# Performance work log

Hardware: AMD Instinct MI355X
Metric: run time of the kernel (lower is better)

Reference implementation:

```python
import jax, jax.numpy as jnp
import numpy as np


def setup_inputs() -> dict:
    key = jax.random.key(0)
    k1, k2 = jax.random.split(key)
    B, C, H = 1024, 1000, 512  # batch, classes, hidden
    y = jax.random.normal(k1, (B, C), dtype=jnp.float32)
    w = jax.random.normal(k2, (C, H), dtype=jnp.float32)
    epsilon = jnp.ones((), dtype=jnp.float32)
    lipschitz = jnp.ones((), dtype=jnp.float32)
    return {"y": y, "w": w, "epsilon": epsilon, "lipschitz": lipschitz}


def reference(y, w, epsilon, lipschitz):
    # y: [B, C] logits; w: [C, H] final-layer weight
    kW = lipschitz * w.T                      # [H, C]
    j = jnp.argmax(y, axis=1)                 # [B]
    y_j = jnp.max(y, axis=1, keepdims=True)   # [B, 1]
    kW_j = kW.T[j]                            # [B, H] gather of argmax column
    kW_ij = kW_j[:, :, None] - kW[None]       # [B, H, C] broadcast difference
    sq = jnp.sum(kW_ij * kW_ij, axis=1)       # [B, C]
    # safe sqrt (value identical; avoids NaN grad at the exact-zero j column)
    K_ij = jnp.where(sq > 0, jnp.sqrt(jnp.where(sq > 0, sq, 1.0)), 0.0)
    y_bot_i = y + epsilon * K_ij              # [B, C]
    y_bot_i = jnp.where(y == y_j, -jnp.inf, y_bot_i)
    y_bot = jnp.max(y_bot_i, axis=1, keepdims=True)  # [B, 1]
    return jnp.concatenate([y, y_bot], axis=1)       # [B, C+1]
```

## Files before the change

### kernel.cpp

```cpp
#include <hip/hip_runtime.h>
#include <math.h>

#define B_SZ 1024
#define C_SZ 1000
#define H_SZ 512


typedef __attribute__((ext_vector_type(8))) short bf16x8;
typedef __attribute__((ext_vector_type(4))) float f32x4;

#define KC 128
#define RS 136

__global__ __launch_bounds__(256) void k_prep(
    const float* __restrict__ y, const float* __restrict__ w,
    int* __restrict__ jv, float* __restrict__ ymax,
    float* __restrict__ wnorm, short* __restrict__ wbf,
    float* __restrict__ out) {
    const int r = blockIdx.x;
    const int tid = threadIdx.x;
    if (r < 250) {
        const int wave = tid >> 6, lane = tid & 63;
        const int c = r * 4 + wave;
        const float* row = w + c * H_SZ;
        float4 a = *(const float4*)(row + lane * 8);
        float4 b = *(const float4*)(row + lane * 8 + 4);
        float f[8] = {a.x, a.y, a.z, a.w, b.x, b.y, b.z, b.w};
        unsigned short u[8];
        float s = 0.f;
#pragma unroll
        for (int i = 0; i < 8; ++i) {
            s += f[i] * f[i];
            unsigned v = __float_as_uint(f[i]);
            v += 0x7fffu + ((v >> 16) & 1u);
            u[i] = (unsigned short)(v >> 16);
        }
        uint4 pk;
        pk.x = (unsigned)u[0] | ((unsigned)u[1] << 16);
        pk.y = (unsigned)u[2] | ((unsigned)u[3] << 16);
        pk.z = (unsigned)u[4] | ((unsigned)u[5] << 16);
        pk.w = (unsigned)u[6] | ((unsigned)u[7] << 16);
        *(uint4*)(wbf + c * H_SZ + lane * 8) = pk;
#pragma unroll
        for (int off = 32; off; off >>= 1) s += __shfl_down(s, off, 64);
        if (lane == 0) wnorm[c] = s;
    } else {
        const int b = r - 250;
        const float* yrow = y + b * C_SZ;
        float* orow = out + b * (C_SZ + 1);
        float best = -INFINITY;
        int bidx = 0x7fffffff;
        if (tid < 250) {
            float4 v = *(const float4*)(yrow + tid * 4);
            float e[4] = {v.x, v.y, v.z, v.w};
#pragma unroll
            for (int i = 0; i < 4; ++i) {
                orow[tid * 4 + i] = e[i];
                if (e[i] > best) { best = e[i]; bidx = tid * 4 + i; }
            }
        }
        const int lane = tid & 63;
#pragma unroll
        for (int off = 32; off; off >>= 1) {
            float ov = __shfl_down(best, off, 64);
            int oi = __shfl_down(bidx, off, 64);
            if (ov > best || (ov == best && oi < bidx)) { best = ov; bidx = oi; }
        }
        __shared__ float sv[4];
        __shared__ int si[4];
        if (lane == 0) { sv[tid >> 6] = best; si[tid >> 6] = bidx; }
        __syncthreads();
        if (tid == 0) {
            float bv = sv[0]; int bi = si[0];
#pragma unroll
            for (int k = 1; k < 4; ++k) {
                if (sv[k] > bv || (sv[k] == bv && si[k] < bi)) { bv = sv[k]; bi = si[k]; }
            }
            jv[b] = bi;
            ymax[b] = bv;
        }
    }
}

__global__ __launch_bounds__(256) void k_main(
    const float* __restrict__ y, const short* __restrict__ wbf,
    const float* __restrict__ eps_p, const float* __restrict__ lip_p,
    const int* __restrict__ jv, const float* __restrict__ ymax,
    const float* __restrict__ wnorm, float* __restrict__ part) {
    __shared__ __align__(16) short As[16 * RS];
    __shared__ __align__(16) short Bs[64 * RS];
    __shared__ int sjv[16];
    __shared__ float snj[16];
    __shared__ float sym[16];
    __shared__ float wred[4][16];

    const int t = threadIdx.x;
    const int wv = t >> 6, lane = t & 63;
    const int col = lane & 15, quad = lane >> 4;
    const int bx = blockIdx.x, by = blockIdx.y;
    const int b0 = by * 16, c0 = bx * 64;

    if (t < 16) {
        int j = jv[b0 + t];
        sjv[t] = j;
        snj[t] = wnorm[j];
        sym[t] = ymax[b0 + t];
    }
    __syncthreads();

    const int arow = t >> 4;
    const int aseg = t & 15;
    const short* ag = wbf + sjv[arow] * H_SZ + aseg * 8;
    int browv[4], bsegv[4];
    const short* bg[4];
#pragma unroll
    for (int p = 0; p < 4; ++p) {
        const int idx = p * 256 + t;
        browv[p] = idx >> 4;
        bsegv[p] = idx & 15;
        int cr = c0 + browv[p];
        if (cr > C_SZ - 1) cr = C_SZ - 1;
        bg[p] = wbf + cr * H_SZ + bsegv[p] * 8;
    }

    uint4 pa = *(const uint4*)ag;
    uint4 pb[4];
#pragma unroll
    for (int p = 0; p < 4; ++p) pb[p] = *(const uint4*)bg[p];

    const short* ard = &As[col * RS + quad * 8];
    const short* brd = &Bs[(wv * 16 + col) * RS + quad * 8];

    f32x4 acc = {0.f, 0.f, 0.f, 0.f};

    for (int ch = 0; ch < 4; ++ch) {
        *(uint4*)&As[arow * RS + aseg * 8] = pa;
#pragma unroll
        for (int p = 0; p < 4; ++p)
            *(uint4*)&Bs[browv[p] * RS + bsegv[p] * 8] = pb[p];
        __syncthreads();
        if (ch < 3) {
            const int go = (ch + 1) * KC;
            pa = *(const uint4*)(ag + go);
#pragma unroll
            for (int p = 0; p < 4; ++p) pb[p] = *(const uint4*)(bg[p] + go);
        }
#pragma unroll
        for (int ks = 0; ks < 4; ++ks) {
            bf16x8 af = *(const bf16x8*)(ard + ks * 32);
            bf16x8 bf = *(const bf16x8*)(brd + ks * 32);
            acc = __builtin_amdgcn_mfma_f32_16x16x32_bf16(af, bf, acc, 0, 0, 0);
        }
        __syncthreads();
    }

    const float eps = *eps_p;
    const float L = *lip_p;
    const float L2 = L * L;
    const int cc = c0 + wv * 16 + col;
    const float nc = wnorm[cc < C_SZ ? cc : C_SZ - 1];
    float rmax[4];
#pragma unroll
    for (int i = 0; i < 4; ++i) {
        const int br = quad * 4 + i;
        const int b = b0 + br;
        float cand = -INFINITY;
        if (cc < C_SZ) {
            const float yv = y[b * C_SZ + cc];
            const float sq = L2 * (snj[br] + nc - 2.0f * acc[i]);
            const float K = sq > 0.f ? sqrtf(sq) : 0.f;
            cand = (yv == sym[br]) ? -INFINITY : yv + eps * K;
        }
        rmax[i] = cand;
    }
#pragma unroll
    for (int off = 8; off; off >>= 1)
#pragma unroll
        for (int i = 0; i < 4; ++i)
            rmax[i] = fmaxf(rmax[i], __shfl_xor(rmax[i], off, 64));
    if (col == 0) {
#pragma unroll
        for (int i = 0; i < 4; ++i) wred[wv][quad * 4 + i] = rmax[i];
    }
    __syncthreads();
    if (t < 16) {
        float m = fmaxf(fmaxf(wred[0][t], wred[1][t]),
                        fmaxf(wred[2][t], wred[3][t]));
        part[bx * B_SZ + b0 + t] = m;
    }
}

__global__ void k_final(const float* __restrict__ part,
                        float* __restrict__ out) {
    int b = blockIdx.x * 256 + threadIdx.x;
    if (b >= B_SZ) return;
    float m = -INFINITY;
#pragma unroll
    for (int s = 0; s < 16; ++s) m = fmaxf(m, part[s * B_SZ + b]);
    out[b * (C_SZ + 1) + C_SZ] = m;
}

extern "C" void kernel_launch(void* const* d_in, const int* in_sizes, int n_in,
                              void* d_out, int out_size, void* d_ws,
                              size_t ws_size, hipStream_t stream) {
    const float* y = (const float*)d_in[0];
    const float* w = (const float*)d_in[1];
    const float* eps = (const float*)d_in[2];
    const float* lip = (const float*)d_in[3];
    float* out = (float*)d_out;

    char* ws = (char*)d_ws;
    int* jv = (int*)ws;
    float* ymax = (float*)(ws + 4096);
    float* wnorm = (float*)(ws + 8192);
    float* part = (float*)(ws + 16384);
    short* wbf = (short*)(ws + 524288);

    k_prep<<<250 + B_SZ, 256, 0, stream>>>(y, w, jv, ymax, wnorm, wbf, out);
    k_main<<<dim3(16, 64), 256, 0, stream>>>(y, wbf, eps, lip, jv, ymax, wnorm,
                                             part);
    k_final<<<(B_SZ + 255) / 256, 256, 0, stream>>>(part, out);
}
```

Before: 86.28 us.

## Fuse prep into main kernel: in-block argmax, fp32 loads with on-the-fly bf16 pack and norms

Drops the separate prep kernel. Each main-kernel block now computes the argmax for its 16 rows directly from y. It loads fp32 weights, converts them to bf16 while staging into shared memory, and accumulates the squared norms of the gathered and column rows in the same loop. The y-to-output copy moves into the final kernel, which also reduces the partial maxima with a wave shuffle. This removes one launch and the bf16/norm workspace round trip, but every block re-reads y rows for the argmax and loads twice as many weight bytes as fp32, with redundant conversion work across blocks.

```diff
diff --git a/kernel.cpp b/kernel.cpp
--- a/kernel.cpp
+++ b/kernel.cpp
@@ -12,86 +12,41 @@
 #define KC 128
 #define RS 136
 
-__global__ __launch_bounds__(256) void k_prep(
+__device__ __forceinline__ uint4 pack8(float4 a, float4 b) {
+    unsigned e[8] = {__float_as_uint(a.x), __float_as_uint(a.y),
+                     __float_as_uint(a.z), __float_as_uint(a.w),
+                     __float_as_uint(b.x), __float_as_uint(b.y),
+                     __float_as_uint(b.z), __float_as_uint(b.w)};
+    unsigned short h[8];
+#pragma unroll
+    for (int i = 0; i < 8; ++i) {
+        unsigned v = e[i];
+        v += 0x7fffu + ((v >> 16) & 1u);
+        h[i] = (unsigned short)(v >> 16);
+    }
+    uint4 p;
+    p.x = (unsigned)h[0] | ((unsigned)h[1] << 16);
+    p.y = (unsigned)h[2] | ((unsigned)h[3] << 16);
+    p.z = (unsigned)h[4] | ((unsigned)h[5] << 16);
+    p.w = (unsigned)h[6] | ((unsigned)h[7] << 16);
+    return p;
+}
+
+__device__ __forceinline__ float sumsq8(float4 a, float4 b) {
+    return a.x * a.x + a.y * a.y + a.z * a.z + a.w * a.w +
+           b.x * b.x + b.y * b.y + b.z * b.z + b.w * b.w;
+}
+
+__global__ __launch_bounds__(256) void k_main(
     const float* __restrict__ y, const float* __restrict__ w,
-    int* __restrict__ jv, float* __restrict__ ymax,
-    float* __restrict__ wnorm, short* __restrict__ wbf,
-    float* __restrict__ out) {
-    const int r = blockIdx.x;
-    const int tid = threadIdx.x;
-    if (r < 250) {
-        const int wave = tid >> 6, lane = tid & 63;
-        const int c = r * 4 + wave;
-        const float* row = w + c * H_SZ;
-        float4 a = *(const float4*)(row + lane * 8);
-        float4 b = *(const float4*)(row + lane * 8 + 4);
-        float f[8] = {a.x, a.y, a.z, a.w, b.x, b.y, b.z, b.w};
-        unsigned short u[8];
-        float s = 0.f;
-#pragma unroll
-        for (int i = 0; i < 8; ++i) {
-            s += f[i] * f[i];
-            unsigned v = __float_as_uint(f[i]);
-            v += 0x7fffu + ((v >> 16) & 1u);
-            u[i] = (unsigned short)(v >> 16);
-        }
-        uint4 pk;
-        pk.x = (unsigned)u[0] | ((unsigned)u[1] << 16);
-        pk.y = (unsigned)u[2] | ((unsigned)u[3] << 16);
-        pk.z = (unsigned)u[4] | ((unsigned)u[5] << 16);
-        pk.w = (unsigned)u[6] | ((unsigned)u[7] << 16);
-        *(uint4*)(wbf + c * H_SZ + lane * 8) = pk;
-#pragma unroll
-        for (int off = 32; off; off >>= 1) s += __shfl_down(s, off, 64);
-        if (lane == 0) wnorm[c] = s;
-    } else {
-        const int b = r - 250;
-        const float* yrow = y + b * C_SZ;
-        float* orow = out + b * (C_SZ + 1);
-        float best = -INFINITY;
-        int bidx = 0x7fffffff;
-        if (tid < 250) {
-            float4 v = *(const float4*)(yrow + tid * 4);
-            float e[4] = {v.x, v.y, v.z, v.w};
-#pragma unroll
-            for (int i = 0; i < 4; ++i) {
-                orow[tid * 4 + i] = e[i];
-                if (e[i] > best) { best = e[i]; bidx = tid * 4 + i; }
-            }
-        }
-        const int lane = tid & 63;
-#pragma unroll
-        for (int off = 32; off; off >>= 1) {
-            float ov = __shfl_down(best, off, 64);
-            int oi = __shfl_down(bidx, off, 64);
-            if (ov > best || (ov == best && oi < bidx)) { best = ov; bidx = oi; }
-        }
-        __shared__ float sv[4];
-        __shared__ int si[4];
-        if (lane == 0) { sv[tid >> 6] = best; si[tid >> 6] = bidx; }
-        __syncthreads();
-        if (tid == 0) {
-            float bv = sv[0]; int bi = si[0];
-#pragma unroll
-            for (int k = 1; k < 4; ++k) {
-                if (sv[k] > bv || (sv[k] == bv && si[k] < bi)) { bv = sv[k]; bi = si[k]; }
-            }
-            jv[b] = bi;
-            ymax[b] = bv;
-        }
-    }
-}
-
-__global__ __launch_bounds__(256) void k_main(
-    const float* __restrict__ y, const short* __restrict__ wbf,
     const float* __restrict__ eps_p, const float* __restrict__ lip_p,
-    const int* __restrict__ jv, const float* __restrict__ ymax,
-    const float* __restrict__ wnorm, float* __restrict__ part) {
+    float* __restrict__ part) {
     __shared__ __align__(16) short As[16 * RS];
     __shared__ __align__(16) short Bs[64 * RS];
     __shared__ int sjv[16];
+    __shared__ float sym[16];
     __shared__ float snj[16];
-    __shared__ float sym[16];
+    __shared__ float snc[64];
     __shared__ float wred[4][16];
 
     const int t = threadIdx.x;
@@ -100,50 +55,81 @@
     const int bx = blockIdx.x, by = blockIdx.y;
     const int b0 = by * 16, c0 = bx * 64;
 
-    if (t < 16) {
-        int j = jv[b0 + t];
-        sjv[t] = j;
-        snj[t] = wnorm[j];
-        sym[t] = ymax[b0 + t];
+    {
+        const int lr = t >> 4, seg = t & 15;
+        const float* yrow = y + (b0 + lr) * C_SZ;
+        float best = -INFINITY;
+        int bidx = 0x7fffffff;
+#pragma unroll
+        for (int i = 0; i < 16; ++i) {
+            const int idx = seg + i * 16;
+            if (idx < 250) {
+                float4 v = *(const float4*)(yrow + idx * 4);
+                float e[4] = {v.x, v.y, v.z, v.w};
+#pragma unroll
+                for (int j = 0; j < 4; ++j) {
+                    if (e[j] > best) { best = e[j]; bidx = idx * 4 + j; }
+                }
+            }
+        }
+#pragma unroll
+        for (int off = 8; off; off >>= 1) {
+            float ov = __shfl_xor(best, off, 64);
+            int oi = __shfl_xor(bidx, off, 64);
+            if (ov > best || (ov == best && oi < bidx)) { best = ov; bidx = oi; }
+        }
+        if (seg == 0) { sjv[lr] = bidx; sym[lr] = best; }
     }
     __syncthreads();
 
     const int arow = t >> 4;
     const int aseg = t & 15;
-    const short* ag = wbf + sjv[arow] * H_SZ + aseg * 8;
-    int browv[4], bsegv[4];
-    const short* bg[4];
+    const float* ag = w + sjv[arow] * H_SZ + aseg * 8;
+    int brow_[4];
+    const float* bg[4];
 #pragma unroll
     for (int p = 0; p < 4; ++p) {
         const int idx = p * 256 + t;
-        browv[p] = idx >> 4;
-        bsegv[p] = idx & 15;
-        int cr = c0 + browv[p];
+        brow_[p] = idx >> 4;
+        int cr = c0 + brow_[p];
         if (cr > C_SZ - 1) cr = C_SZ - 1;
-        bg[p] = wbf + cr * H_SZ + bsegv[p] * 8;
-    }
-
-    uint4 pa = *(const uint4*)ag;
-    uint4 pb[4];
-#pragma unroll
-    for (int p = 0; p < 4; ++p) pb[p] = *(const uint4*)bg[p];
+        bg[p] = w + cr * H_SZ + aseg * 8;
+    }
+
+    float4 pa0 = *(const float4*)ag;
+    float4 pa1 = *(const float4*)(ag + 4);
+    float4 pb0[4], pb1[4];
+#pragma unroll
+    for (int p = 0; p < 4; ++p) {
+        pb0[p] = *(const float4*)bg[p];
+        pb1[p] = *(const float4*)(bg[p] + 4);
+    }
 
     const short* ard = &As[col * RS + quad * 8];
     const short* brd = &Bs[(wv * 16 + col) * RS + quad * 8];
 
     f32x4 acc = {0.f, 0.f, 0.f, 0.f};
+    float na = 0.f;
+    float nb[4] = {0.f, 0.f, 0.f, 0.f};
 
     for (int ch = 0; ch < 4; ++ch) {
-        *(uint4*)&As[arow * RS + aseg * 8] = pa;
-#pragma unroll
-        for (int p = 0; p < 4; ++p)
-            *(uint4*)&Bs[browv[p] * RS + bsegv[p] * 8] = pb[p];
+        na += sumsq8(pa0, pa1);
+        *(uint4*)&As[arow * RS + aseg * 8] = pack8(pa0, pa1);
+#pragma unroll
+        for (int p = 0; p < 4; ++p) {
+            nb[p] += sumsq8(pb0[p], pb1[p]);
+            *(uint4*)&Bs[brow_[p] * RS + aseg * 8] = pack8(pb0[p], pb1[p]);
+        }
         __syncthreads();
         if (ch < 3) {
             const int go = (ch + 1) * KC;
-            pa = *(const uint4*)(ag + go);
-#pragma unroll
-            for (int p = 0; p < 4; ++p) pb[p] = *(const uint4*)(bg[p] + go);
+            pa0 = *(const float4*)(ag + go);
+            pa1 = *(const float4*)(ag + go + 4);
+#pragma unroll
+            for (int p = 0; p < 4; ++p) {
+                pb0[p] = *(const float4*)(bg[p] + go);
+                pb1[p] = *(const float4*)(bg[p] + go + 4);
+            }
         }
 #pragma unroll
         for (int ks = 0; ks < 4; ++ks) {
@@ -154,11 +140,25 @@
         __syncthreads();
     }
 
+#pragma unroll
+    for (int off = 1; off < 16; off <<= 1) na += __shfl_xor(na, off, 64);
+#pragma unroll
+    for (int p = 0; p < 4; ++p)
+#pragma unroll
+        for (int off = 1; off < 16; off <<= 1)
+            nb[p] += __shfl_xor(nb[p], off, 64);
+    if (aseg == 0) {
+        snj[arow] = na;
+#pragma unroll
+        for (int p = 0; p < 4; ++p) snc[brow_[p]] = nb[p];
+    }
+    __syncthreads();
+
     const float eps = *eps_p;
     const float L = *lip_p;
     const float L2 = L * L;
     const int cc = c0 + wv * 16 + col;
-    const float nc = wnorm[cc < C_SZ ? cc : C_SZ - 1];
+    const float nc = snc[wv * 16 + col];
     float rmax[4];
 #pragma unroll
     for (int i = 0; i < 4; ++i) {
@@ -186,18 +186,32 @@
     if (t < 16) {
         float m = fmaxf(fmaxf(wred[0][t], wred[1][t]),
                         fmaxf(wred[2][t], wred[3][t]));
-        part[bx * B_SZ + b0 + t] = m;
-    }
-}
-
-__global__ void k_final(const float* __restrict__ part,
-                        float* __restrict__ out) {
-    int b = blockIdx.x * 256 + threadIdx.x;
-    if (b >= B_SZ) return;
+        __hip_atomic_store(&part[bx * B_SZ + b0 + t], m, __ATOMIC_RELAXED,
+                           __HIP_MEMORY_SCOPE_AGENT);
+    }
+}
+
+__global__ __launch_bounds__(256) void k_final(const float* __restrict__ y,
+                                               float* __restrict__ part,
+                                               float* __restrict__ out) {
+    const int t = threadIdx.x;
+    const int wv = t >> 6, lane = t & 63;
+    const int b = blockIdx.x * 4 + wv;
+    const float* yrow = y + b * C_SZ;
+    float* orow = out + b * (C_SZ + 1);
+#pragma unroll
+    for (int i = 0; i < 4; ++i) {
+        const int idx = i * 64 + lane;
+        if (idx < 250)
+            *(float4*)(orow + idx * 4) = *(const float4*)(yrow + idx * 4);
+    }
     float m = -INFINITY;
-#pragma unroll
-    for (int s = 0; s < 16; ++s) m = fmaxf(m, part[s * B_SZ + b]);
-    out[b * (C_SZ + 1) + C_SZ] = m;
+    if (lane < 16)
+        m = __hip_atomic_load(&part[lane * B_SZ + b], __ATOMIC_RELAXED,
+                              __HIP_MEMORY_SCOPE_AGENT);
+#pragma unroll
+    for (int off = 8; off; off >>= 1) m = fmaxf(m, __shfl_xor(m, off, 64));
+    if (lane == 0) orow[C_SZ] = m;
 }
 
 extern "C" void kernel_launch(void* const* d_in, const int* in_sizes, int n_in,
@@ -208,16 +222,8 @@
     const float* eps = (const float*)d_in[2];
     const float* lip = (const float*)d_in[3];
     float* out = (float*)d_out;
-
-    char* ws = (char*)d_ws;
-    int* jv = (int*)ws;
-    float* ymax = (float*)(ws + 4096);
-    float* wnorm = (float*)(ws + 8192);
-    float* part = (float*)(ws + 16384);
-    short* wbf = (short*)(ws + 524288);
-
-    k_prep<<<250 + B_SZ, 256, 0, stream>>>(y, w, jv, ymax, wnorm, wbf, out);
-    k_main<<<dim3(16, 64), 256, 0, stream>>>(y, wbf, eps, lip, jv, ymax, wnorm,
-                                             part);
-    k_final<<<(B_SZ + 255) / 256, 256, 0, stream>>>(part, out);
-}
+    float* part = (float*)d_ws;
+
+    k_main<<<dim3(16, 64), 256, 0, stream>>>(y, w, eps, lip, part);
+    k_final<<<B_SZ / 4, 256, 0, stream>>>(y, part, out);
+}
```

Measured after the change: 82.80 us. 1.04x faster.
